# Optimization experiments

Measured on AMD Instinct MI355X. Metric: run time of the kernel, lower is better.

## Reference

```python
import jax, jax.numpy as jnp
import numpy as np
import math

IN_CH = 256
CH = 128
SCALE = math.sqrt(CH)
TEMPERATURE = 1.0


def setup_inputs() -> dict:
    key = jax.random.key(0)
    ks = jax.random.split(key, 9)
    B, C, H, W = 8, IN_CH, 56, 56
    x = jax.random.normal(ks[0], (B, C, H, W), dtype=jnp.float32)
    s_in = 1.0 / math.sqrt(IN_CH)
    s_ch = 1.0 / math.sqrt(CH)
    wq = jax.random.uniform(ks[1], (CH, IN_CH), minval=-s_in, maxval=s_in)
    bq = jax.random.uniform(ks[2], (CH,), minval=-s_in, maxval=s_in)
    wk = jax.random.uniform(ks[3], (CH, IN_CH), minval=-s_in, maxval=s_in)
    bk = jax.random.uniform(ks[4], (CH,), minval=-s_in, maxval=s_in)
    wv = jax.random.uniform(ks[5], (CH, IN_CH), minval=-s_in, maxval=s_in)
    bv = jax.random.uniform(ks[6], (CH,), minval=-s_in, maxval=s_in)
    wo = jax.random.uniform(ks[7], (IN_CH, CH), minval=-s_ch, maxval=s_ch)
    bo = jax.random.uniform(ks[8], (IN_CH,), minval=-s_ch, maxval=s_ch)
    return {"x": x, "wq": wq, "bq": bq, "wk": wk, "bk": bk,
            "wv": wv, "bv": bv, "wo": wo, "bo": bo}


def reference(x, wq, bq, wk, bk, wv, bv, wo, bo):
    B, C, H, W = x.shape
    N = H * W
    xf = x.reshape(B, C, N)  # flatten spatial; 1x1 conv == channel matmul
    q = jnp.einsum('oc,bcn->bon', wq, xf) + bq[None, :, None]  # (B,CH,N)
    k = jnp.einsum('oc,bcn->bon', wk, xf) + bk[None, :, None]
    v = jnp.einsum('oc,bcn->bon', wv, xf) + bv[None, :, None]
    # similarity map (B, N, N): query positions x key positions
    sim = jnp.einsum('bcn,bcm->bnm', q, k) / (SCALE * TEMPERATURE)
    attn = jax.nn.softmax(sim, axis=2)
    out = jnp.einsum('bnm,bcm->bnc', attn, v)  # (B, N, CH)
    out = jnp.einsum('oc,bnc->bon', wo, out) + bo[None, :, None]  # (B,IN_CH,N)
    return x + out.reshape(B, C, H, W)
```

## Files before the change

### kernel.cpp

```cpp
#include <hip/hip_runtime.h>
#include <hip/hip_bf16.h>
#include <math.h>

#define NPOS 3136
#define NB   8
#define SCALE_INV 0.08838834764831845f
#define SM_OFS 8.0f

typedef __attribute__((ext_vector_type(8))) short shortx8;
typedef __attribute__((ext_vector_type(4))) short shortx4;
typedef __attribute__((ext_vector_type(4))) float f32x4;

__device__ __forceinline__ unsigned short f2bf(float f) {
    unsigned int i = __builtin_bit_cast(unsigned int, f);
    i += 0x7FFFu + ((i >> 16) & 1u);
    return (unsigned short)(i >> 16);
}
__device__ __forceinline__ unsigned short f2bf_fast(float f) {
    return __builtin_bit_cast(unsigned short, __float2bfloat16(f));
}
__device__ __forceinline__ void gll16(const unsigned short* g, unsigned short* l) {
    __builtin_amdgcn_global_load_lds((const __attribute__((address_space(1))) void*)g,
                                     (__attribute__((address_space(3))) void*)l, 16, 0, 0);
}

__global__ __launch_bounds__(256) void cast_w(
    const float* __restrict__ wq, const float* __restrict__ wk,
    const float* __restrict__ wv, const float* __restrict__ wo,
    unsigned short* __restrict__ Wb)
{
    const int sel = blockIdx.y;
    const float* src = (sel == 0) ? wq : (sel == 1) ? wk : (sel == 2) ? wv : wo;
    const float sc = (sel == 0) ? SCALE_INV : 1.0f;
    unsigned short* dst = Wb + sel * 32768;
    int i0 = (blockIdx.x * 256 + threadIdx.x) * 8;
    #pragma unroll
    for (int e = 0; e < 8; ++e) dst[i0 + e] = f2bf(src[i0 + e] * sc);
}

__global__ __launch_bounds__(256) void cast_xT(
    const float* __restrict__ x, unsigned short* __restrict__ xT)
{
    const int b = blockIdx.z, c0 = blockIdx.y * 64, n0 = blockIdx.x * 64;
    __shared__ unsigned short Ls[64 * 66];
    const int t = threadIdx.x;
    {
        int r = t >> 2, q4 = t & 3;
        const float* src = x + ((size_t)b * 256 + c0 + r) * NPOS + n0 + q4 * 16;
        #pragma unroll
        for (int i = 0; i < 16; ++i) Ls[r * 66 + q4 * 16 + i] = f2bf(src[i]);
    }
    __syncthreads();
    {
        int j = t >> 2, h4 = t & 3;
        shortx8 v0, v1;
        #pragma unroll
        for (int i = 0; i < 8; ++i) v0[i] = (short)Ls[(h4 * 16 + i) * 66 + j];
        #pragma unroll
        for (int i = 0; i < 8; ++i) v1[i] = (short)Ls[(h4 * 16 + 8 + i) * 66 + j];
        unsigned short* dst = xT + ((size_t)b * NPOS + n0 + j) * 256 + c0 + h4 * 16;
        *reinterpret_cast<shortx8*>(dst) = v0;
        *reinterpret_cast<shortx8*>(dst + 8) = v1;
    }
}

__global__ __launch_bounds__(256) void qkv_mfma(
    const unsigned short* __restrict__ xT,
    const unsigned short* __restrict__ Wb,
    const float* __restrict__ bq, const float* __restrict__ bk, const float* __restrict__ bv,
    unsigned short* __restrict__ qT, unsigned short* __restrict__ kT,
    unsigned short* __restrict__ vC)
{
    const int b = blockIdx.z, sel = blockIdx.y, n0 = blockIdx.x * 64;
    const int t = threadIdx.x, lane = t & 63, wave = t >> 6;
    const int l16 = lane & 15, lhi = lane >> 4;
    __shared__ __align__(16) unsigned short Wt[128 * 128];
    __shared__ __align__(16) unsigned short Xt[64 * 128];
    const unsigned short* Wsel = Wb + sel * 32768;
    const float* bias = (sel == 0) ? bq : (sel == 1) ? bk : bv;

    f32x4 acc[2][4];
    #pragma unroll
    for (int ab = 0; ab < 2; ++ab)
        #pragma unroll
        for (int nb = 0; nb < 4; ++nb) acc[ab][nb] = f32x4{0.f, 0.f, 0.f, 0.f};

    for (int ks0 = 0; ks0 < 2; ++ks0) {
        const int k0 = ks0 * 128;
        __syncthreads();
        #pragma unroll
        for (int i = 0; i < 8; ++i) {
            int c = (wave * 8 + i) * 64 + lane;
            int row = c >> 4, cin = (c & 15) ^ (row & 7);
            gll16(Wsel + (size_t)row * 256 + k0 + cin * 8, &Wt[0] + (wave * 8 + i) * 512);
        }
        #pragma unroll
        for (int i = 0; i < 4; ++i) {
            int c = (wave * 4 + i) * 64 + lane;
            int row = c >> 4, cin = (c & 15) ^ (row & 7);
            gll16(xT + ((size_t)b * NPOS + n0 + row) * 256 + k0 + cin * 8,
                  &Xt[0] + (wave * 4 + i) * 512);
        }
        __syncthreads();
        #pragma unroll
        for (int ks = 0; ks < 4; ++ks) {
            shortx8 aW[2];
            #pragma unroll
            for (int ab = 0; ab < 2; ++ab) {
                int row = wave * 32 + ab * 16 + l16;
                int idx = (row * 128 + ks * 32 + lhi * 8) ^ ((row & 7) << 3);
                aW[ab] = *reinterpret_cast<const shortx8*>(Wt + idx);
            }
            #pragma unroll
            for (int nb = 0; nb < 4; ++nb) {
                int row = nb * 16 + l16;
                int idx = (row * 128 + ks * 32 + lhi * 8) ^ ((row & 7) << 3);
                shortx8 bX = *reinterpret_cast<const shortx8*>(Xt + idx);
                acc[0][nb] = __builtin_amdgcn_mfma_f32_16x16x32_bf16(aW[0], bX, acc[0][nb], 0, 0, 0);
                acc[1][nb] = __builtin_amdgcn_mfma_f32_16x16x32_bf16(aW[1], bX, acc[1][nb], 0, 0, 0);
            }
        }
    }
    const int strip = wave * 32;
    if (sel < 2) {
        unsigned short* dst0 = ((sel == 0) ? qT : kT) + (size_t)b * NPOS * 128;
        const float bsc = (sel == 0) ? SCALE_INV : 1.0f;
        #pragma unroll
        for (int ab = 0; ab < 2; ++ab) {
            int ocb = strip + ab * 16 + lhi * 4;
            float bb[4];
            #pragma unroll
            for (int j = 0; j < 4; ++j) bb[j] = bias[ocb + j] * bsc;
            #pragma unroll
            for (int nb = 0; nb < 4; ++nb) {
                int n = n0 + nb * 16 + l16;
                shortx4 u;
                #pragma unroll
                for (int j = 0; j < 4; ++j) u[j] = (short)f2bf(acc[ab][nb][j] + bb[j]);
                *reinterpret_cast<shortx4*>(dst0 + (size_t)n * 128 + ocb) = u;
            }
        }
    } else {
        #pragma unroll
        for (int ab = 0; ab < 2; ++ab)
            #pragma unroll
            for (int j = 0; j < 4; ++j) {
                int oc = strip + ab * 16 + lhi * 4 + j;
                float bb = bias[oc];
                unsigned short* dst = vC + ((size_t)b * 128 + oc) * NPOS + n0;
                #pragma unroll
                for (int nb = 0; nb < 4; ++nb)
                    dst[nb * 16 + l16] = f2bf(acc[ab][nb][j] + bb);
            }
    }
}

__global__ __launch_bounds__(256) void attn_kernel(
    const unsigned short* __restrict__ qT,
    const unsigned short* __restrict__ kT,
    const unsigned short* __restrict__ vC,
    unsigned short* __restrict__ ao)
{
    const int b = blockIdx.y, n0 = blockIdx.x * 64;
    const int t = threadIdx.x, lane = t & 63, wave = t >> 6;
    const int l16 = lane & 15, lhi = lane >> 4;

    __shared__ __align__(16) unsigned short KsB[2][64 * 128];
    __shared__ __align__(16) unsigned short VsB[2][128 * 64];
    __shared__ __align__(16) unsigned short Ps[4][16 * 64];

    shortx8 aQ[4];
    {
        const unsigned short* qp = qT + ((size_t)b * NPOS + n0 + wave * 16 + l16) * 128 + lhi * 8;
        #pragma unroll
        for (int kk = 0; kk < 4; ++kk)
            aQ[kk] = *reinterpret_cast<const shortx8*>(qp + kk * 32);
    }

    const unsigned short* kSrc[4];
    const unsigned short* vSrc[4];
    unsigned kDst[4];
    #pragma unroll
    for (int i = 0; i < 4; ++i) {
        int c = (wave * 4 + i) * 64 + lane;
        int rK = c >> 4, cK = (c & 15) ^ (rK & 7);
        kSrc[i] = kT + ((size_t)b * NPOS + rK) * 128 + cK * 8;
        int rV = c >> 3, cV = (c & 7) ^ (rV & 7);
        vSrc[i] = vC + ((size_t)b * 128 + rV) * NPOS + cV * 8;
        kDst[i] = (wave * 4 + i) * 512;
    }

    unsigned kIdx[4][4], vIdx[8][2], pW[4][4], pR[2];
    #pragma unroll
    for (int cb = 0; cb < 4; ++cb) {
        int row = cb * 16 + l16;
        #pragma unroll
        for (int kk = 0; kk < 4; ++kk)
            kIdx[cb][kk] = (row * 128 + kk * 32 + lhi * 8) ^ ((row & 7) << 3);
    }
    #pragma unroll
    for (int ob = 0; ob < 8; ++ob) {
        int row = ob * 16 + l16;
        #pragma unroll
        for (int ks = 0; ks < 2; ++ks)
            vIdx[ob][ks] = (row * 64 + ks * 32 + lhi * 8) ^ ((row & 7) << 3);
    }
    #pragma unroll
    for (int j = 0; j < 4; ++j) {
        int r = lhi * 4 + j;
        #pragma unroll
        for (int cb = 0; cb < 4; ++cb)
            pW[j][cb] = (r * 64 + cb * 16 + l16) ^ ((r & 7) << 3);
    }
    #pragma unroll
    for (int ks = 0; ks < 2; ++ks)
        pR[ks] = (l16 * 64 + ks * 32 + lhi * 8) ^ ((l16 & 7) << 3);

    float lrow[4] = {0.f, 0.f, 0.f, 0.f};
    f32x4 o[8];
    #pragma unroll
    for (int ob = 0; ob < 8; ++ob) o[ob] = f32x4{0.f, 0.f, 0.f, 0.f};

    #pragma unroll
    for (int i = 0; i < 4; ++i) {
        gll16(kSrc[i], &KsB[0][0] + kDst[i]);
        gll16(vSrc[i], &VsB[0][0] + kDst[i]);
    }
    __syncthreads();

    int cur = 0;
    for (int kt = 0; kt < NPOS / 64; ++kt) {
        if (kt + 1 < NPOS / 64) {
            const int m1 = (kt + 1) * 64;
            #pragma unroll
            for (int i = 0; i < 4; ++i) {
                gll16(kSrc[i] + (size_t)m1 * 128, &KsB[cur ^ 1][0] + kDst[i]);
                gll16(vSrc[i] + m1, &VsB[cur ^ 1][0] + kDst[i]);
            }
        }
        const unsigned short* Ks = &KsB[cur][0];
        const unsigned short* Vs = &VsB[cur][0];

        f32x4 s[4];
        #pragma unroll
        for (int cb = 0; cb < 4; ++cb) {
            s[cb] = f32x4{0.f, 0.f, 0.f, 0.f};
            #pragma unroll
            for (int kk = 0; kk < 4; ++kk) {
                shortx8 bK = *reinterpret_cast<const shortx8*>(Ks + kIdx[cb][kk]);
                s[cb] = __builtin_amdgcn_mfma_f32_16x16x32_bf16(aQ[kk], bK, s[cb], 0, 0, 0);
            }
        }
        #pragma unroll
        for (int cb = 0; cb < 4; ++cb)
            #pragma unroll
            for (int j = 0; j < 4; ++j) {
                float p = __expf(s[cb][j] - SM_OFS);
                lrow[j] += p;
                Ps[wave][pW[j][cb]] = f2bf_fast(p);
            }
        shortx8 aP[2];
        #pragma unroll
        for (int ks = 0; ks < 2; ++ks)
            aP[ks] = *reinterpret_cast<const shortx8*>(&Ps[wave][0] + pR[ks]);
        #pragma unroll
        for (int ob = 0; ob < 8; ++ob)
            #pragma unroll
            for (int ks = 0; ks < 2; ++ks) {
                shortx8 bV = *reinterpret_cast<const shortx8*>(Vs + vIdx[ob][ks]);
                o[ob] = __builtin_amdgcn_mfma_f32_16x16x32_bf16(aP[ks], bV, o[ob], 0, 0, 0);
            }
        __syncthreads();
        cur ^= 1;
    }

    #pragma unroll
    for (int j = 0; j < 4; ++j) {
        float v = lrow[j];
        #pragma unroll
        for (int off = 1; off <= 8; off <<= 1) v += __shfl_xor(v, off);
        lrow[j] = 1.f / v;
    }
    unsigned short* aob = ao + ((size_t)b * NPOS + n0 + wave * 16) * 128;
    #pragma unroll
    for (int ob = 0; ob < 8; ++ob)
        #pragma unroll
        for (int j = 0; j < 4; ++j) {
            int q = lhi * 4 + j;
            aob[(size_t)q * 128 + ob * 16 + l16] = f2bf_fast(o[ob][j] * lrow[j]);
        }
}

__global__ __launch_bounds__(256) void out_proj(
    const float* __restrict__ x,
    const unsigned short* __restrict__ Wb,
    const float* __restrict__ bo,
    const unsigned short* __restrict__ ao,
    float* __restrict__ y)
{
    const int b = blockIdx.y, n0 = blockIdx.x * 64;
    const int t = threadIdx.x, lane = t & 63, wave = t >> 6;
    const int l16 = lane & 15, lhi = lane >> 4;
    __shared__ __align__(16) unsigned short Wt[256 * 128];
    __shared__ __align__(16) unsigned short At[64 * 128];
    const unsigned short* wo = Wb + 98304;

    #pragma unroll
    for (int i = 0; i < 16; ++i) {
        int c = (wave * 16 + i) * 64 + lane;
        int row = c >> 4, cin = (c & 15) ^ (row & 7);
        gll16(wo + (size_t)row * 128 + cin * 8, &Wt[0] + (wave * 16 + i) * 512);
    }
    #pragma unroll
    for (int i = 0; i < 4; ++i) {
        int c = (wave * 4 + i) * 64 + lane;
        int row = c >> 4, cin = (c & 15) ^ (row & 7);
        gll16(ao + ((size_t)b * NPOS + n0 + row) * 128 + cin * 8, &At[0] + (wave * 4 + i) * 512);
    }
    __syncthreads();

    f32x4 acc[4][4];
    #pragma unroll
    for (int ab = 0; ab < 4; ++ab)
        #pragma unroll
        for (int nb = 0; nb < 4; ++nb) acc[ab][nb] = f32x4{0.f, 0.f, 0.f, 0.f};

    const int strip = wave * 64;
    #pragma unroll
    for (int ks = 0; ks < 4; ++ks) {
        shortx8 aW[4];
        #pragma unroll
        for (int ab = 0; ab < 4; ++ab) {
            int row = strip + ab * 16 + l16;
            int idx = (row * 128 + ks * 32 + lhi * 8) ^ ((row & 7) << 3);
            aW[ab] = *reinterpret_cast<const shortx8*>(Wt + idx);
        }
        #pragma unroll
        for (int nb = 0; nb < 4; ++nb) {
            int row = nb * 16 + l16;
            int idx = (row * 128 + ks * 32 + lhi * 8) ^ ((row & 7) << 3);
            shortx8 bA = *reinterpret_cast<const shortx8*>(At + idx);
            #pragma unroll
            for (int ab = 0; ab < 4; ++ab)
                acc[ab][nb] = __builtin_amdgcn_mfma_f32_16x16x32_bf16(aW[ab], bA, acc[ab][nb], 0, 0, 0);
        }
    }

    #pragma unroll
    for (int ab = 0; ab < 4; ++ab)
        #pragma unroll
        for (int j = 0; j < 4; ++j) {
            int oc = strip + ab * 16 + lhi * 4 + j;
            float bb = bo[oc];
            const float* xr = x + ((size_t)b * 256 + oc) * NPOS + n0;
            float* yr = y + ((size_t)b * 256 + oc) * NPOS + n0;
            #pragma unroll
            for (int nb = 0; nb < 4; ++nb) {
                int n = nb * 16 + l16;
                yr[n] = xr[n] + bb + acc[ab][nb][j];
            }
        }
}

extern "C" void kernel_launch(void* const* d_in, const int* in_sizes, int n_in,
                              void* d_out, int out_size, void* d_ws, size_t ws_size,
                              hipStream_t stream)
{
    const float* x  = (const float*)d_in[0];
    const float* wq = (const float*)d_in[1];
    const float* bq = (const float*)d_in[2];
    const float* wk = (const float*)d_in[3];
    const float* bk = (const float*)d_in[4];
    const float* wv = (const float*)d_in[5];
    const float* bv = (const float*)d_in[6];
    const float* wo = (const float*)d_in[7];
    const float* bo = (const float*)d_in[8];
    float* y = (float*)d_out;

    const size_t sz = (size_t)NB * NPOS * 128;
    unsigned short* qT = (unsigned short*)d_ws;
    unsigned short* kT = qT + sz;
    unsigned short* vC = kT + sz;
    unsigned short* xT = vC + sz;
    unsigned short* ao = xT;
    unsigned short* Wb = xT + 2 * sz;

    cast_w  <<<dim3(16, 4),       256, 0, stream>>>(wq, wk, wv, wo, Wb);
    cast_xT <<<dim3(49, 4, NB),   256, 0, stream>>>(x, xT);
    qkv_mfma<<<dim3(49, 3, NB),   256, 0, stream>>>(xT, Wb, bq, bk, bv, qT, kT, vC);
    attn_kernel<<<dim3(49, NB),   256, 0, stream>>>(qT, kT, vC, ao);
    out_proj<<<dim3(49, NB),      256, 0, stream>>>(x, Wb, bo, ao, y);
}
```

Measured before the change: 141.0 us.

## Split attention waves into 32-query by 32-key sub-tiles with cross-wave reduction

Each wave now handles 32 query rows against half of the 64-key tile instead of 16 queries against all keys. Every K and V fragment read from LDS then feeds two MFMAs, halving LDS fragment traffic per MFMA. The partial outputs and row sums from the two key-half waves are combined through shared memory at the end. The cost is twice the accumulator registers per wave, which may lower occupancy, plus an extra synchronisation and LDS reduction step.

```diff
diff --git a/kernel.cpp b/kernel.cpp
--- a/kernel.cpp
+++ b/kernel.cpp
@@ -164,17 +164,20 @@
     const int b = blockIdx.y, n0 = blockIdx.x * 64;
     const int t = threadIdx.x, lane = t & 63, wave = t >> 6;
     const int l16 = lane & 15, lhi = lane >> 4;
+    const int qsub = wave >> 1, khalf = wave & 1;
 
     __shared__ __align__(16) unsigned short KsB[2][64 * 128];
     __shared__ __align__(16) unsigned short VsB[2][128 * 64];
-    __shared__ __align__(16) unsigned short Ps[4][16 * 64];
-
-    shortx8 aQ[4];
-    {
-        const unsigned short* qp = qT + ((size_t)b * NPOS + n0 + wave * 16 + l16) * 128 + lhi * 8;
+    __shared__ __align__(16) unsigned short Ps[4][32 * 32];
+
+    shortx8 aQ[2][4];
+    #pragma unroll
+    for (int qq = 0; qq < 2; ++qq) {
+        const unsigned short* qp =
+            qT + ((size_t)b * NPOS + n0 + qsub * 32 + qq * 16 + l16) * 128 + lhi * 8;
         #pragma unroll
         for (int kk = 0; kk < 4; ++kk)
-            aQ[kk] = *reinterpret_cast<const shortx8*>(qp + kk * 32);
+            aQ[qq][kk] = *reinterpret_cast<const shortx8*>(qp + kk * 32);
     }
 
     const unsigned short* kSrc[4];
@@ -190,10 +193,10 @@
         kDst[i] = (wave * 4 + i) * 512;
     }
 
-    unsigned kIdx[4][4], vIdx[8][2], pW[4][4], pR[2];
-    #pragma unroll
-    for (int cb = 0; cb < 4; ++cb) {
-        int row = cb * 16 + l16;
+    unsigned kIdx[2][4], vIdx[8], pR[2];
+    #pragma unroll
+    for (int cb = 0; cb < 2; ++cb) {
+        int row = khalf * 32 + cb * 16 + l16;
         #pragma unroll
         for (int kk = 0; kk < 4; ++kk)
             kIdx[cb][kk] = (row * 128 + kk * 32 + lhi * 8) ^ ((row & 7) << 3);
@@ -201,25 +204,21 @@
     #pragma unroll
     for (int ob = 0; ob < 8; ++ob) {
         int row = ob * 16 + l16;
-        #pragma unroll
-        for (int ks = 0; ks < 2; ++ks)
-            vIdx[ob][ks] = (row * 64 + ks * 32 + lhi * 8) ^ ((row & 7) << 3);
-    }
-    #pragma unroll
-    for (int j = 0; j < 4; ++j) {
-        int r = lhi * 4 + j;
-        #pragma unroll
-        for (int cb = 0; cb < 4; ++cb)
-            pW[j][cb] = (r * 64 + cb * 16 + l16) ^ ((r & 7) << 3);
-    }
-    #pragma unroll
-    for (int ks = 0; ks < 2; ++ks)
-        pR[ks] = (l16 * 64 + ks * 32 + lhi * 8) ^ ((l16 & 7) << 3);
-
-    float lrow[4] = {0.f, 0.f, 0.f, 0.f};
-    f32x4 o[8];
-    #pragma unroll
-    for (int ob = 0; ob < 8; ++ob) o[ob] = f32x4{0.f, 0.f, 0.f, 0.f};
+        vIdx[ob] = (row * 64 + khalf * 32 + lhi * 8) ^ ((row & 7) << 3);
+    }
+    #pragma unroll
+    for (int qq = 0; qq < 2; ++qq) {
+        int r = qq * 16 + l16;
+        int chunk = lhi ^ ((l16 & 3) ^ ((l16 >> 2) & 3));
+        pR[qq] = r * 32 + chunk * 8;
+    }
+
+    float lrow[2][4] = {{0.f, 0.f, 0.f, 0.f}, {0.f, 0.f, 0.f, 0.f}};
+    f32x4 o[2][8];
+    #pragma unroll
+    for (int qq = 0; qq < 2; ++qq)
+        #pragma unroll
+        for (int ob = 0; ob < 8; ++ob) o[qq][ob] = f32x4{0.f, 0.f, 0.f, 0.f};
 
     #pragma unroll
     for (int i = 0; i < 4; ++i) {
@@ -241,54 +240,84 @@
         const unsigned short* Ks = &KsB[cur][0];
         const unsigned short* Vs = &VsB[cur][0];
 
-        f32x4 s[4];
-        #pragma unroll
-        for (int cb = 0; cb < 4; ++cb) {
-            s[cb] = f32x4{0.f, 0.f, 0.f, 0.f};
+        f32x4 s[2][2];
+        #pragma unroll
+        for (int cb = 0; cb < 2; ++cb) {
+            s[0][cb] = f32x4{0.f, 0.f, 0.f, 0.f};
+            s[1][cb] = f32x4{0.f, 0.f, 0.f, 0.f};
             #pragma unroll
             for (int kk = 0; kk < 4; ++kk) {
                 shortx8 bK = *reinterpret_cast<const shortx8*>(Ks + kIdx[cb][kk]);
-                s[cb] = __builtin_amdgcn_mfma_f32_16x16x32_bf16(aQ[kk], bK, s[cb], 0, 0, 0);
-            }
-        }
-        #pragma unroll
-        for (int cb = 0; cb < 4; ++cb)
-            #pragma unroll
-            for (int j = 0; j < 4; ++j) {
-                float p = __expf(s[cb][j] - SM_OFS);
-                lrow[j] += p;
-                Ps[wave][pW[j][cb]] = f2bf_fast(p);
-            }
+                s[0][cb] = __builtin_amdgcn_mfma_f32_16x16x32_bf16(aQ[0][kk], bK, s[0][cb], 0, 0, 0);
+                s[1][cb] = __builtin_amdgcn_mfma_f32_16x16x32_bf16(aQ[1][kk], bK, s[1][cb], 0, 0, 0);
+            }
+        }
+        #pragma unroll
+        for (int qq = 0; qq < 2; ++qq)
+            #pragma unroll
+            for (int cb = 0; cb < 2; ++cb)
+                #pragma unroll
+                for (int j = 0; j < 4; ++j) {
+                    float p = __expf(s[qq][cb][j] - SM_OFS);
+                    lrow[qq][j] += p;
+                    int r = qq * 16 + lhi * 4 + j;
+                    int chunk = ((cb * 2 + (l16 >> 3)) ^ j ^ lhi);
+                    Ps[wave][r * 32 + chunk * 8 + (l16 & 7)] = f2bf_fast(p);
+                }
         shortx8 aP[2];
         #pragma unroll
-        for (int ks = 0; ks < 2; ++ks)
-            aP[ks] = *reinterpret_cast<const shortx8*>(&Ps[wave][0] + pR[ks]);
-        #pragma unroll
-        for (int ob = 0; ob < 8; ++ob)
-            #pragma unroll
-            for (int ks = 0; ks < 2; ++ks) {
-                shortx8 bV = *reinterpret_cast<const shortx8*>(Vs + vIdx[ob][ks]);
-                o[ob] = __builtin_amdgcn_mfma_f32_16x16x32_bf16(aP[ks], bV, o[ob], 0, 0, 0);
-            }
+        for (int qq = 0; qq < 2; ++qq)
+            aP[qq] = *reinterpret_cast<const shortx8*>(&Ps[wave][0] + pR[qq]);
+        #pragma unroll
+        for (int ob = 0; ob < 8; ++ob) {
+            shortx8 bV = *reinterpret_cast<const shortx8*>(Vs + vIdx[ob]);
+            o[0][ob] = __builtin_amdgcn_mfma_f32_16x16x32_bf16(aP[0], bV, o[0][ob], 0, 0, 0);
+            o[1][ob] = __builtin_amdgcn_mfma_f32_16x16x32_bf16(aP[1], bV, o[1][ob], 0, 0, 0);
+        }
         __syncthreads();
         cur ^= 1;
     }
 
-    #pragma unroll
-    for (int j = 0; j < 4; ++j) {
-        float v = lrow[j];
-        #pragma unroll
-        for (int off = 1; off <= 8; off <<= 1) v += __shfl_xor(v, off);
-        lrow[j] = 1.f / v;
-    }
-    unsigned short* aob = ao + ((size_t)b * NPOS + n0 + wave * 16) * 128;
-    #pragma unroll
-    for (int ob = 0; ob < 8; ++ob)
-        #pragma unroll
-        for (int j = 0; j < 4; ++j) {
-            int q = lhi * 4 + j;
-            aob[(size_t)q * 128 + ob * 16 + l16] = f2bf_fast(o[ob][j] * lrow[j]);
-        }
+    float* Om = reinterpret_cast<float*>(&KsB[0][0]);
+    float* Lr = reinterpret_cast<float*>(&VsB[0][0]);
+    if (khalf == 1) {
+        #pragma unroll
+        for (int qq = 0; qq < 2; ++qq)
+            #pragma unroll
+            for (int ob = 0; ob < 8; ++ob)
+                *reinterpret_cast<f32x4*>(&Om[(((qsub * 2 + qq) * 8 + ob) * 64 + lane) * 4]) = o[qq][ob];
+        #pragma unroll
+        for (int qq = 0; qq < 2; ++qq)
+            #pragma unroll
+            for (int j = 0; j < 4; ++j)
+                Lr[((qsub * 2 + qq) * 4 + j) * 64 + lane] = lrow[qq][j];
+    }
+    __syncthreads();
+    if (khalf == 0) {
+        float inv[2][4];
+        #pragma unroll
+        for (int qq = 0; qq < 2; ++qq)
+            #pragma unroll
+            for (int j = 0; j < 4; ++j) {
+                float v = lrow[qq][j] + Lr[((qsub * 2 + qq) * 4 + j) * 64 + lane];
+                #pragma unroll
+                for (int off = 1; off <= 8; off <<= 1) v += __shfl_xor(v, off);
+                inv[qq][j] = 1.f / v;
+            }
+        unsigned short* aob = ao + ((size_t)b * NPOS + n0 + qsub * 32) * 128;
+        #pragma unroll
+        for (int qq = 0; qq < 2; ++qq)
+            #pragma unroll
+            for (int ob = 0; ob < 8; ++ob) {
+                f32x4 oo = o[qq][ob];
+                oo += *reinterpret_cast<const f32x4*>(&Om[(((qsub * 2 + qq) * 8 + ob) * 64 + lane) * 4]);
+                #pragma unroll
+                for (int j = 0; j < 4; ++j) {
+                    int q = qq * 16 + lhi * 4 + j;
+                    aob[(size_t)q * 128 + ob * 16 + l16] = f2bf_fast(oo[j] * inv[qq][j]);
+                }
+            }
+    }
 }
 
 __global__ __launch_bounds__(256) void out_proj(
```

Measured after the change: 135.9 us. 3.6% less time.

## Restructure attention to 32x32 MFMA with in-register P and split-K waves

Applied to the files above, without the earlier changes.

Rewrites the attention kernel to use 32x32x16 bf16 MFMA, computing S transposed so the exp'd probabilities can be packed in registers and fed straight into the PV MFMA. This removes the per-wave LDS round trip for P. Waves are split across key halves and their partial outputs are reduced through LDS at the end. Softmax now uses exp2 with log2e folded into the Q scale, and the row-sum normalization is deferred to the output projection through a new workspace buffer. In exchange the kernel needs an extra epilogue reduction with LDS traffic and syncs, and output precision shifts slightly because ao is stored unnormalized.

```diff
diff --git a/kernel.cpp b/kernel.cpp
--- a/kernel.cpp
+++ b/kernel.cpp
@@ -4,21 +4,23 @@
 
 #define NPOS 3136
 #define NB   8
-#define SCALE_INV 0.08838834764831845f
-#define SM_OFS 8.0f
+#define LOG2E 1.44269504088896f
+#define QSCALE (0.08838834764831845f * LOG2E)
+#define OFS2  11.54156032711168f
 
 typedef __attribute__((ext_vector_type(8))) short shortx8;
 typedef __attribute__((ext_vector_type(4))) short shortx4;
 typedef __attribute__((ext_vector_type(4))) float f32x4;
+typedef __attribute__((ext_vector_type(16))) float f32x16;
+typedef __attribute__((ext_vector_type(4))) unsigned int uint4v;
+
+struct S8pair { shortx4 lo, hi; };
 
 __device__ __forceinline__ unsigned short f2bf(float f) {
     unsigned int i = __builtin_bit_cast(unsigned int, f);
     i += 0x7FFFu + ((i >> 16) & 1u);
     return (unsigned short)(i >> 16);
 }
-__device__ __forceinline__ unsigned short f2bf_fast(float f) {
-    return __builtin_bit_cast(unsigned short, __float2bfloat16(f));
-}
 __device__ __forceinline__ void gll16(const unsigned short* g, unsigned short* l) {
     __builtin_amdgcn_global_load_lds((const __attribute__((address_space(1))) void*)g,
                                      (__attribute__((address_space(3))) void*)l, 16, 0, 0);
@@ -31,7 +33,7 @@
 {
     const int sel = blockIdx.y;
     const float* src = (sel == 0) ? wq : (sel == 1) ? wk : (sel == 2) ? wv : wo;
-    const float sc = (sel == 0) ? SCALE_INV : 1.0f;
+    const float sc = (sel == 0) ? QSCALE : 1.0f;
     unsigned short* dst = Wb + sel * 32768;
     int i0 = (blockIdx.x * 256 + threadIdx.x) * 8;
     #pragma unroll
@@ -124,7 +126,7 @@
     const int strip = wave * 32;
     if (sel < 2) {
         unsigned short* dst0 = ((sel == 0) ? qT : kT) + (size_t)b * NPOS * 128;
-        const float bsc = (sel == 0) ? SCALE_INV : 1.0f;
+        const float bsc = (sel == 0) ? QSCALE : 1.0f;
         #pragma unroll
         for (int ab = 0; ab < 2; ++ab) {
             int ocb = strip + ab * 16 + lhi * 4;
@@ -159,72 +161,67 @@
     const unsigned short* __restrict__ qT,
     const unsigned short* __restrict__ kT,
     const unsigned short* __restrict__ vC,
-    unsigned short* __restrict__ ao)
+    unsigned short* __restrict__ ao,
+    float* __restrict__ lrG)
 {
     const int b = blockIdx.y, n0 = blockIdx.x * 64;
     const int t = threadIdx.x, lane = t & 63, wave = t >> 6;
-    const int l16 = lane & 15, lhi = lane >> 4;
+    const int l31 = lane & 31, h = lane >> 5;
+    const int qsub = wave >> 1, kh = wave & 1;
 
     __shared__ __align__(16) unsigned short KsB[2][64 * 128];
     __shared__ __align__(16) unsigned short VsB[2][128 * 64];
-    __shared__ __align__(16) unsigned short Ps[4][16 * 64];
-
-    shortx8 aQ[4];
+
+    shortx8 aQ[8];
     {
-        const unsigned short* qp = qT + ((size_t)b * NPOS + n0 + wave * 16 + l16) * 128 + lhi * 8;
-        #pragma unroll
-        for (int kk = 0; kk < 4; ++kk)
-            aQ[kk] = *reinterpret_cast<const shortx8*>(qp + kk * 32);
+        const unsigned short* qp = qT + ((size_t)b * NPOS + n0 + qsub * 32 + l31) * 128 + h * 8;
+        #pragma unroll
+        for (int kk = 0; kk < 8; ++kk)
+            aQ[kk] = *reinterpret_cast<const shortx8*>(qp + kk * 16);
     }
 
     const unsigned short* kSrc[4];
     const unsigned short* vSrc[4];
-    unsigned kDst[4];
+    unsigned sDst[4];
     #pragma unroll
     for (int i = 0; i < 4; ++i) {
         int c = (wave * 4 + i) * 64 + lane;
-        int rK = c >> 4, cK = (c & 15) ^ (rK & 7);
+        int rK = c >> 4, cK = (c & 15) ^ (rK & 15);
         kSrc[i] = kT + ((size_t)b * NPOS + rK) * 128 + cK * 8;
         int rV = c >> 3, cV = (c & 7) ^ (rV & 7);
         vSrc[i] = vC + ((size_t)b * 128 + rV) * NPOS + cV * 8;
-        kDst[i] = (wave * 4 + i) * 512;
-    }
-
-    unsigned kIdx[4][4], vIdx[8][2], pW[4][4], pR[2];
-    #pragma unroll
-    for (int cb = 0; cb < 4; ++cb) {
-        int row = cb * 16 + l16;
-        #pragma unroll
-        for (int kk = 0; kk < 4; ++kk)
-            kIdx[cb][kk] = (row * 128 + kk * 32 + lhi * 8) ^ ((row & 7) << 3);
-    }
-    #pragma unroll
-    for (int ob = 0; ob < 8; ++ob) {
-        int row = ob * 16 + l16;
+        sDst[i] = (wave * 4 + i) * 512;
+    }
+
+    unsigned kIdx[8];
+    {
+        int rowK = kh * 32 + l31;
+        #pragma unroll
+        for (int kk = 0; kk < 8; ++kk)
+            kIdx[kk] = rowK * 128 + (((kk * 2 + h) ^ (rowK & 15)) * 8);
+    }
+    unsigned vIdx[4][2][2];
+    #pragma unroll
+    for (int ob = 0; ob < 4; ++ob) {
+        int rowV = ob * 32 + l31;
         #pragma unroll
         for (int ks = 0; ks < 2; ++ks)
-            vIdx[ob][ks] = (row * 64 + ks * 32 + lhi * 8) ^ ((row & 7) << 3);
-    }
-    #pragma unroll
-    for (int j = 0; j < 4; ++j) {
-        int r = lhi * 4 + j;
-        #pragma unroll
-        for (int cb = 0; cb < 4; ++cb)
-            pW[j][cb] = (r * 64 + cb * 16 + l16) ^ ((r & 7) << 3);
-    }
-    #pragma unroll
-    for (int ks = 0; ks < 2; ++ks)
-        pR[ks] = (l16 * 64 + ks * 32 + lhi * 8) ^ ((l16 & 7) << 3);
-
-    float lrow[4] = {0.f, 0.f, 0.f, 0.f};
-    f32x4 o[8];
-    #pragma unroll
-    for (int ob = 0; ob < 8; ++ob) o[ob] = f32x4{0.f, 0.f, 0.f, 0.f};
+            #pragma unroll
+            for (int rr = 0; rr < 2; ++rr)
+                vIdx[ob][ks][rr] = rowV * 64 + (((kh * 4 + ks * 2 + rr) ^ (rowV & 7)) * 8) + h * 4;
+    }
+
+    f32x16 o[4];
+    #pragma unroll
+    for (int ob = 0; ob < 4; ++ob)
+        #pragma unroll
+        for (int r = 0; r < 16; ++r) o[ob][r] = 0.f;
+    float lrP = 0.f;
 
     #pragma unroll
     for (int i = 0; i < 4; ++i) {
-        gll16(kSrc[i], &KsB[0][0] + kDst[i]);
-        gll16(vSrc[i], &VsB[0][0] + kDst[i]);
+        gll16(kSrc[i], &KsB[0][0] + sDst[i]);
+        gll16(vSrc[i], &VsB[0][0] + sDst[i]);
     }
     __syncthreads();
 
@@ -234,61 +231,87 @@
             const int m1 = (kt + 1) * 64;
             #pragma unroll
             for (int i = 0; i < 4; ++i) {
-                gll16(kSrc[i] + (size_t)m1 * 128, &KsB[cur ^ 1][0] + kDst[i]);
-                gll16(vSrc[i] + m1, &VsB[cur ^ 1][0] + kDst[i]);
+                gll16(kSrc[i] + (size_t)m1 * 128, &KsB[cur ^ 1][0] + sDst[i]);
+                gll16(vSrc[i] + m1, &VsB[cur ^ 1][0] + sDst[i]);
             }
         }
         const unsigned short* Ks = &KsB[cur][0];
         const unsigned short* Vs = &VsB[cur][0];
 
-        f32x4 s[4];
-        #pragma unroll
-        for (int cb = 0; cb < 4; ++cb) {
-            s[cb] = f32x4{0.f, 0.f, 0.f, 0.f};
-            #pragma unroll
-            for (int kk = 0; kk < 4; ++kk) {
-                shortx8 bK = *reinterpret_cast<const shortx8*>(Ks + kIdx[cb][kk]);
-                s[cb] = __builtin_amdgcn_mfma_f32_16x16x32_bf16(aQ[kk], bK, s[cb], 0, 0, 0);
-            }
-        }
-        #pragma unroll
-        for (int cb = 0; cb < 4; ++cb)
-            #pragma unroll
-            for (int j = 0; j < 4; ++j) {
-                float p = __expf(s[cb][j] - SM_OFS);
-                lrow[j] += p;
-                Ps[wave][pW[j][cb]] = f2bf_fast(p);
-            }
-        shortx8 aP[2];
-        #pragma unroll
-        for (int ks = 0; ks < 2; ++ks)
-            aP[ks] = *reinterpret_cast<const shortx8*>(&Ps[wave][0] + pR[ks]);
-        #pragma unroll
-        for (int ob = 0; ob < 8; ++ob)
-            #pragma unroll
-            for (int ks = 0; ks < 2; ++ks) {
-                shortx8 bV = *reinterpret_cast<const shortx8*>(Vs + vIdx[ob][ks]);
-                o[ob] = __builtin_amdgcn_mfma_f32_16x16x32_bf16(aP[ks], bV, o[ob], 0, 0, 0);
-            }
+        f32x16 sA, sB;
+        #pragma unroll
+        for (int r = 0; r < 16; ++r) { sA[r] = 0.f; sB[r] = 0.f; }
+        #pragma unroll
+        for (int kk = 0; kk < 8; kk += 2) {
+            shortx8 k0 = *reinterpret_cast<const shortx8*>(Ks + kIdx[kk]);
+            shortx8 k1 = *reinterpret_cast<const shortx8*>(Ks + kIdx[kk + 1]);
+            sA = __builtin_amdgcn_mfma_f32_32x32x16_bf16(k0, aQ[kk], sA, 0, 0, 0);
+            sB = __builtin_amdgcn_mfma_f32_32x32x16_bf16(k1, aQ[kk + 1], sB, 0, 0, 0);
+        }
+
+        unsigned pk[8];
+        #pragma unroll
+        for (int g = 0; g < 4; ++g) {
+            float p0 = exp2f(sA[g * 4 + 0] + sB[g * 4 + 0] - OFS2);
+            float p1 = exp2f(sA[g * 4 + 1] + sB[g * 4 + 1] - OFS2);
+            float p2 = exp2f(sA[g * 4 + 2] + sB[g * 4 + 2] - OFS2);
+            float p3 = exp2f(sA[g * 4 + 3] + sB[g * 4 + 3] - OFS2);
+            lrP += (p0 + p1) + (p2 + p3);
+            asm("v_cvt_pk_bf16_f32 %0, %1, %2" : "=v"(pk[g * 2 + 0]) : "v"(p0), "v"(p1));
+            asm("v_cvt_pk_bf16_f32 %0, %1, %2" : "=v"(pk[g * 2 + 1]) : "v"(p2), "v"(p3));
+        }
+
+        #pragma unroll
+        for (int ks = 0; ks < 2; ++ks) {
+            uint4v pv = {pk[ks * 4 + 0], pk[ks * 4 + 1], pk[ks * 4 + 2], pk[ks * 4 + 3]};
+            shortx8 PA = __builtin_bit_cast(shortx8, pv);
+            #pragma unroll
+            for (int ob = 0; ob < 4; ++ob) {
+                shortx4 lo = *reinterpret_cast<const shortx4*>(Vs + vIdx[ob][ks][0]);
+                shortx4 hi = *reinterpret_cast<const shortx4*>(Vs + vIdx[ob][ks][1]);
+                shortx8 bV = __builtin_bit_cast(shortx8, S8pair{lo, hi});
+                o[ob] = __builtin_amdgcn_mfma_f32_32x32x16_bf16(PA, bV, o[ob], 0, 0, 0);
+            }
+        }
         __syncthreads();
         cur ^= 1;
     }
 
-    #pragma unroll
-    for (int j = 0; j < 4; ++j) {
-        float v = lrow[j];
-        #pragma unroll
-        for (int off = 1; off <= 8; off <<= 1) v += __shfl_xor(v, off);
-        lrow[j] = 1.f / v;
-    }
-    unsigned short* aob = ao + ((size_t)b * NPOS + n0 + wave * 16) * 128;
-    #pragma unroll
-    for (int ob = 0; ob < 8; ++ob)
-        #pragma unroll
-        for (int j = 0; j < 4; ++j) {
-            int q = lhi * 4 + j;
-            aob[(size_t)q * 128 + ob * 16 + l16] = f2bf_fast(o[ob][j] * lrow[j]);
-        }
+    float lr2 = lrP + __shfl_xor(lrP, 32);
+    float* Om = reinterpret_cast<float*>(&KsB[0][0]);
+    float* lrS = reinterpret_cast<float*>(&VsB[1][0]);
+    unsigned short* Oo = &VsB[0][0];
+
+    if (kh == 1) {
+        #pragma unroll
+        for (int ob = 0; ob < 4; ++ob)
+            #pragma unroll
+            for (int r = 0; r < 16; ++r) {
+                int q = qsub * 32 + (r & 3) + 8 * (r >> 2) + 4 * h;
+                Om[q * 128 + ob * 32 + l31] = o[ob][r];
+            }
+        if (lane < 32) lrS[qsub * 32 + l31] = lr2;
+    }
+    __syncthreads();
+    if (kh == 0) {
+        #pragma unroll
+        for (int ob = 0; ob < 4; ++ob)
+            #pragma unroll
+            for (int r = 0; r < 16; ++r) {
+                int q = qsub * 32 + (r & 3) + 8 * (r >> 2) + 4 * h;
+                int idx = q * 128 + ob * 32 + l31;
+                Oo[idx] = f2bf(o[ob][r] + Om[idx]);
+            }
+        if (lane < 32)
+            lrG[(size_t)b * NPOS + n0 + qsub * 32 + l31] = lr2 + lrS[qsub * 32 + l31];
+    }
+    __syncthreads();
+    {
+        const shortx8* src = reinterpret_cast<const shortx8*>(Oo);
+        shortx8* dst = reinterpret_cast<shortx8*>(ao + ((size_t)b * NPOS + n0) * 128);
+        #pragma unroll
+        for (int i = 0; i < 4; ++i) dst[t + 256 * i] = src[t + 256 * i];
+    }
 }
 
 __global__ __launch_bounds__(256) void out_proj(
@@ -296,6 +319,7 @@
     const unsigned short* __restrict__ Wb,
     const float* __restrict__ bo,
     const unsigned short* __restrict__ ao,
+    const float* __restrict__ lrG,
     float* __restrict__ y)
 {
     const int b = blockIdx.y, n0 = blockIdx.x * 64;
@@ -346,6 +370,11 @@
         }
     }
 
+    float inv[4];
+    #pragma unroll
+    for (int nb = 0; nb < 4; ++nb)
+        inv[nb] = 1.0f / lrG[(size_t)b * NPOS + n0 + nb * 16 + l16];
+
     #pragma unroll
     for (int ab = 0; ab < 4; ++ab)
         #pragma unroll
@@ -357,7 +386,7 @@
             #pragma unroll
             for (int nb = 0; nb < 4; ++nb) {
                 int n = nb * 16 + l16;
-                yr[n] = xr[n] + bb + acc[ab][nb][j];
+                yr[n] = xr[n] + bb + acc[ab][nb][j] * inv[nb];
             }
         }
 }
@@ -384,10 +413,11 @@
     unsigned short* xT = vC + sz;
     unsigned short* ao = xT;
     unsigned short* Wb = xT + 2 * sz;
+    float* lrG = (float*)(Wb + 131072);
 
     cast_w  <<<dim3(16, 4),       256, 0, stream>>>(wq, wk, wv, wo, Wb);
     cast_xT <<<dim3(49, 4, NB),   256, 0, stream>>>(x, xT);
     qkv_mfma<<<dim3(49, 3, NB),   256, 0, stream>>>(xT, Wb, bq, bk, bv, qT, kT, vC);
-    attn_kernel<<<dim3(49, NB),   256, 0, stream>>>(qT, kT, vC, ao);
-    out_proj<<<dim3(49, NB),      256, 0, stream>>>(x, Wb, bo, ao, y);
-}
+    attn_kernel<<<dim3(49, NB),   256, 0, stream>>>(qT, kT, vC, ao, lrG);
+    out_proj<<<dim3(49, NB),      256, 0, stream>>>(x, Wb, bo, ao, lrG, y);
+}
```

After: 130.1 us. 1.08x faster.
